# Optimization experiments

Hardware: AMD Instinct MI355X
Metric: run time of the kernel (lower is better)

## Reference

```python
import jax, jax.numpy as jnp
import numpy as np

B, C, H, W, NH = 8, 192, 128, 128, 6  # batch, channels, height, width, heads


def setup_inputs() -> dict:
    key = jax.random.key(0)
    ks = jax.random.split(key, 5)
    return {
        "x": jax.random.normal(ks[0], (B, C, H, W), jnp.float32),
        "w_qkv": jax.random.normal(ks[1], (3 * C, 1, 3, 3), jnp.float32) * 0.1,  # grouped conv, groups=C
        "b_qkv": jax.random.normal(ks[2], (3 * C,), jnp.float32) * 0.1,
        "temperature": jnp.ones((NH, 1, 1), jnp.float32),
        "w_out": jax.random.normal(ks[3], (C, C), jnp.float32) * 0.05,  # 1x1 conv as dense
        "b_out": jax.random.normal(ks[4], (C,), jnp.float32) * 0.05,
    }


def reference(x, w_qkv, b_qkv, temperature, w_out, b_out):
    b, c, h, w = x.shape
    nh = temperature.shape[0]
    # grouped 3x3 conv (groups = in_ch), padding=1
    qkv = jax.lax.conv_general_dilated(
        x, w_qkv, window_strides=(1, 1), padding=[(1, 1), (1, 1)],
        feature_group_count=c, dimension_numbers=("NCHW", "OIHW", "NCHW"),
    ) + b_qkv[None, :, None, None]
    q, k, v = jnp.split(qkv, 3, axis=1)  # each [b, c, h, w]

    def to_heads(t):
        return t.reshape(b, nh, c // nh, h * w)  # b head c (h w)

    q, k, v = to_heads(q), to_heads(k), to_heads(v)
    eps = 1e-12  # F.normalize default
    q = q / jnp.maximum(jnp.linalg.norm(q, axis=-1, keepdims=True), eps)
    k = k / jnp.maximum(jnp.linalg.norm(k, axis=-1, keepdims=True), eps)
    attn = jnp.einsum("bhcn,bhdn->bhcd", q, k) * temperature[None]  # [b, nh, c/nh, c/nh]
    attn = jax.nn.softmax(attn, axis=-1)
    out = jnp.einsum("bhcd,bhdn->bhcn", attn, v).reshape(b, c, h, w)
    out = jnp.einsum("oc,bchw->bohw", w_out, out) + b_out[None, :, None, None]
    return out
```

## Files before the change

### kernel.cpp

```cpp
#include <hip/hip_runtime.h>
#include <hip/hip_bf16.h>

constexpr int B   = 8;
constexpr int Cc  = 192;
constexpr int H   = 128;
constexpr int Wd  = 128;
constexpr int NH  = 6;
constexpr int HD  = 32;
constexpr int HW  = H * Wd;

typedef short s16x8 __attribute__((ext_vector_type(8)));
typedef float f32x16 __attribute__((ext_vector_type(16)));

constexpr size_t OFF_V    = 0;
constexpr size_t OFF_ATTN = 50331648ULL;
constexpr size_t OFF_SSQ  = OFF_ATTN + 196608ULL;
constexpr size_t OFF_ZERO = OFF_SSQ + 12288ULL;
constexpr size_t OFF_M    = OFF_ZERO + 256ULL;
constexpr int    N_ZERO   = (196608 + 12288 + 256) / 4;

__device__ inline unsigned short f2bf(float f) {
    __hip_bfloat16 h = __float2bfloat16(f);
    return *(unsigned short*)&h;
}

__global__ void zero_kernel(float* __restrict__ p, int n) {
    int i = blockIdx.x * 256 + threadIdx.x;
    if (i < n) p[i] = 0.f;
}

#define AS1C(p) ((const __attribute__((address_space(1))) void*)(p))
#define AS3(p)  ((__attribute__((address_space(3))) void*)(p))


__device__ __forceinline__ void ld6(const float* __restrict__ base, int r,
                                    int q8, float (&e)[6]) {
    const float* p = base + r * 40 + q8 * 4;
    float4 a = *(const float4*)p;
    float4 bq = *(const float4*)(p + 4);
    float2 cd = *(const float2*)(p + 8);
    e[0] = a.w; e[1] = bq.x; e[2] = bq.y; e[3] = bq.z; e[4] = bq.w; e[5] = cd.x;
}

__device__ __forceinline__ float conv_lds(
    const float* __restrict__ base, const float (&wr)[9], float br,
    int q8, int ch, unsigned short* __restrict__ frag)
{
    float rv[3][6];
    ld6(base, 0, q8, rv[0]);
    ld6(base, 1, q8, rv[1]);
    float ss = 0.f;
#pragma unroll
    for (int y = 0; y < 4; ++y) {
        ld6(base, y + 2, q8, rv[(y + 2) % 3]);
        const float* r0 = rv[y % 3];
        const float* r1 = rv[(y + 1) % 3];
        const float* r2 = rv[(y + 2) % 3];
        float o[4];
#pragma unroll
        for (int xx = 0; xx < 4; ++xx) {
            o[xx] = br
                + wr[0] * r0[xx] + wr[1] * r0[xx + 1] + wr[2] * r0[xx + 2]
                + wr[3] * r1[xx] + wr[4] * r1[xx + 1] + wr[5] * r1[xx + 2]
                + wr[6] * r2[xx] + wr[7] * r2[xx + 1] + wr[8] * r2[xx + 2];
        }
        ss += o[0] * o[0] + o[1] * o[1] + o[2] * o[2] + o[3] * o[3];
        ushort4 pk = make_ushort4(f2bf(o[0]), f2bf(o[1]), f2bf(o[2]), f2bf(o[3]));
        int g = 4 * y + (q8 >> 1);
        *(ushort4*)(frag + ((g * 32 + ch) << 3) + ((q8 & 1) << 2)) = pk;
    }
    return ss;
}

__global__ __launch_bounds__(256, 2) void fused_conv_qk(
    const float* __restrict__ x, const float* __restrict__ w,
    const float* __restrict__ bias, float* __restrict__ ssq,
    float* __restrict__ attn, const float* __restrict__ zbuf)
{
    const int tile = blockIdx.x, h = blockIdx.y, b = blockIdx.z;
    const int y0  = tile * 4;
    const int tid = threadIdx.x;
    const int ch  = tid >> 3, q8 = tid & 7;
    const int lane = tid & 63, wv = tid >> 6;
    const int m = lane & 31, hf = lane >> 5;

    __shared__ float xs[2][5760];
    __shared__ unsigned short qs[16 * 32 * 8];
    __shared__ unsigned short ks[16 * 32 * 8];

    const int gq0 = (h * 32) / 3;
    const int ncq = (h * 32 + 31) / 3 - gq0 + 1;
    const int gl  = (h * 32 + ch) / 3 - gq0;

    const int ocq = h * HD + ch;
    float wq[9], wk[9];
#pragma unroll
    for (int t = 0; t < 9; ++t) {
        wq[t] = w[(size_t)ocq * 9 + t];
        wk[t] = w[(size_t)(Cc + ocq) * 9 + t];
    }
    const float bq = bias[ocq], bk = bias[Cc + ocq];

    const float* sp[6];
    int cb[6];
    int i4[6];
    bool act[6];
#pragma unroll
    for (int j = 0; j < 6; ++j) {
        int i = tid + 256 * j;
        act[j] = (i < 1440);
        if (act[j]) {
            int t   = i / 720;
            int jj  = i - t * 720;
            int c   = jj / 60;
            int rem = jj - c * 60;
            int r   = rem / 10;
            int c4  = rem - r * 10;
            int cg  = (c < ncq) ? c : (ncq - 1);
            int gch = t * 64 + gq0 + cg;
            int y   = y0 - 1 + r;
            sp[j] = (y >= 0 && y < H)
                  ? x + ((size_t)b * Cc + gch) * HW + (size_t)y * Wd : nullptr;
            cb[j] = c4 * 4 - 4;
            i4[j] = i * 4;
        } else { sp[j] = nullptr; cb[j] = 0; i4[j] = 0; }
    }

    f32x16 acc;
#pragma unroll
    for (int i = 0; i < 16; ++i) acc[i] = 0.f;
    float ssq_a = 0.f, ssk_a = 0.f;

#pragma unroll
    for (int j = 0; j < 6; ++j) {
        if (!act[j]) continue;
        int col = cb[j];
        const float* src = (sp[j] != nullptr && (unsigned)col <= 124u)
                         ? sp[j] + col : zbuf;
        __builtin_amdgcn_global_load_lds(AS1C(src), AS3(&xs[0][i4[j]]), 16, 0, 0);
    }

#pragma unroll 1
    for (int s = 0; s < 4; ++s) {
        float* cur = xs[s & 1];
        __syncthreads();

        if (s < 3) {
            float* nxt = xs[(s + 1) & 1];
#pragma unroll
            for (int j = 0; j < 6; ++j) {
                if (!act[j]) continue;
                int col = (s + 1) * 32 + cb[j];
                const float* src = (sp[j] != nullptr && (unsigned)col <= 124u)
                                 ? sp[j] + col : zbuf;
                __builtin_amdgcn_global_load_lds(AS1C(src), AS3(&nxt[i4[j]]), 16, 0, 0);
            }
        }

        ssq_a += conv_lds(cur + gl * 240, wq, bq, q8, ch, qs);
        ssk_a += conv_lds(cur + 2880 + gl * 240, wk, bk, q8, ch, ks);
        __syncthreads();

#pragma unroll
        for (int cc = 0; cc < 2; ++cc) {
            int g = (wv * 2 + cc) * 2 + hf;
            s16x8 qa = *(const s16x8*)&qs[(g * 32 + m) << 3];
            s16x8 kb = *(const s16x8*)&ks[(g * 32 + m) << 3];
            acc = __builtin_amdgcn_mfma_f32_32x32x16_bf16(qa, kb, acc, 0, 0, 0);
        }
    }

    __syncthreads();
    float* sacc = (float*)qs;
    for (int i = tid; i < 1024; i += 256) sacc[i] = 0.f;
    __syncthreads();
#pragma unroll
    for (int r = 0; r < 16; ++r) {
        int row = (r & 3) + 8 * (r >> 2) + 4 * hf;
        atomicAdd(&sacc[row * 32 + m], acc[r]);
    }
    __syncthreads();
    float* ap = attn + (size_t)(b * NH + h) * 1024;
    for (int i = tid; i < 1024; i += 256) atomicAdd(&ap[i], sacc[i]);

    for (int off = 4; off; off >>= 1) {
        ssq_a += __shfl_down(ssq_a, off, 8);
        ssk_a += __shfl_down(ssk_a, off, 8);
    }
    if (q8 == 0) {
        atomicAdd(&ssq[b * Cc + ocq], ssq_a);
        atomicAdd(&ssq[B * Cc + b * Cc + ocq], ssk_a);
    }
}

constexpr int TS = 16;

__global__ __launch_bounds__(256) void conv_v(
    const float* __restrict__ x, const float* __restrict__ w,
    const float* __restrict__ bias, unsigned short* __restrict__ vws)
{
    int tile = blockIdx.x;
    int gv   = blockIdx.y;
    int b    = blockIdx.z;
    int y0   = tile * TS;

    __shared__ float sm[TS + 2][132];

    const float* xp = x + ((size_t)b * Cc + 128 + gv) * HW;
    for (int i = threadIdx.x; i < (TS + 2) * 32; i += 256) {
        int r = i >> 5, c4 = (i & 31) * 4;
        int y = y0 - 1 + r;
        if (y >= 0 && y < H) {
            float4 v4 = *(const float4*)(xp + (size_t)y * Wd + c4);
            sm[r][c4 + 1] = v4.x; sm[r][c4 + 2] = v4.y;
            sm[r][c4 + 3] = v4.z; sm[r][c4 + 4] = v4.w;
        } else {
            sm[r][c4 + 1] = 0.f; sm[r][c4 + 2] = 0.f;
            sm[r][c4 + 3] = 0.f; sm[r][c4 + 4] = 0.f;
        }
    }
    for (int i = threadIdx.x; i < (TS + 2) * 2; i += 256) {
        int r = i >> 1;
        sm[r][(i & 1) ? 129 : 0] = 0.f;
    }
    __syncthreads();

    float wreg[3][9], breg[3];
    for (int j = 0; j < 3; ++j) {
        const float* wp = w + (size_t)(2 * Cc + 3 * gv + j) * 9;
#pragma unroll
        for (int t = 0; t < 9; ++t) wreg[j][t] = wp[t];
        breg[j] = bias[2 * Cc + 3 * gv + j];
    }

    int xq = (threadIdx.x & 31) * 4;
    int ys = threadIdx.x >> 5;

    for (int yy = ys; yy < TS; yy += 8) {
        float rvv[3][6];
        for (int r = 0; r < 3; ++r) {
            float4 a4 = *(const float4*)&sm[yy + r][xq];
            float2 a2 = *(const float2*)&sm[yy + r][xq + 4];
            rvv[r][0] = a4.x; rvv[r][1] = a4.y; rvv[r][2] = a4.z;
            rvv[r][3] = a4.w; rvv[r][4] = a2.x; rvv[r][5] = a2.y;
        }
        for (int j = 0; j < 3; ++j) {
            unsigned short pk[4];
            for (int xx = 0; xx < 4; ++xx) {
                float s = breg[j]
                    + wreg[j][0] * rvv[0][xx] + wreg[j][1] * rvv[0][xx + 1] + wreg[j][2] * rvv[0][xx + 2]
                    + wreg[j][3] * rvv[1][xx] + wreg[j][4] * rvv[1][xx + 1] + wreg[j][5] * rvv[1][xx + 2]
                    + wreg[j][6] * rvv[2][xx] + wreg[j][7] * rvv[2][xx + 1] + wreg[j][8] * rvv[2][xx + 2];
                pk[xx] = f2bf(s);
            }
            unsigned short* op = vws + ((size_t)b * Cc + 3 * gv + j) * HW
                                     + (size_t)(y0 + yy) * Wd + xq;
            *(ushort4*)op = make_ushort4(pk[0], pk[1], pk[2], pk[3]);
        }
    }
}

__global__ void softmax_attn(float* __restrict__ attn,
                             const float* __restrict__ ssq,
                             const float* __restrict__ temp)
{
    int h = blockIdx.x % NH, b = blockIdx.x / NH;
    __shared__ float nk[32];
    if (threadIdx.x < 32)
        nk[threadIdx.x] = fmaxf(sqrtf(ssq[B * Cc + b * Cc + h * 32 + threadIdx.x]), 1e-12f);
    __syncthreads();
    int c = threadIdx.x;
    if (c >= 32) return;
    float nq = fmaxf(sqrtf(ssq[b * Cc + h * 32 + c]), 1e-12f);
    float t = temp[h];
    float* ap = attn + ((size_t)(b * NH + h) * 32 + c) * 32;
    float row[32];
    float mx = -1e30f;
    for (int d = 0; d < 32; ++d) {
        float v = ap[d] / (nq * nk[d]) * t;
        row[d] = v;
        mx = fmaxf(mx, v);
    }
    float sum = 0.f;
    for (int d = 0; d < 32; ++d) { row[d] = expf(row[d] - mx); sum += row[d]; }
    float inv = 1.f / sum;
    for (int d = 0; d < 32; ++d) ap[d] = row[d] * inv;
}

__global__ __launch_bounds__(256) void make_m(
    const float* __restrict__ attn, const float* __restrict__ w_out,
    unsigned short* __restrict__ M)
{
    int h = blockIdx.x, b = blockIdx.y;
    __shared__ float as[32][33];
    for (int i = threadIdx.x; i < 1024; i += 256)
        as[i / 32][i % 32] = attn[(size_t)((b * NH + h) * 32 + i / 32) * 32 + i % 32];
    __syncthreads();
    for (int i = threadIdx.x; i < Cc * 32; i += 256) {
        int o = i / 32, d = i % 32;
        const float* wp = w_out + (size_t)o * Cc + h * 32;
        float s = 0.f;
        for (int cp = 0; cp < 32; ++cp) s += wp[cp] * as[cp][d];
        M[((size_t)b * Cc + o) * Cc + h * 32 + d] = f2bf(s);
    }
}

constexpr int BN = 128;

__global__ __launch_bounds__(256) void out_gemm(
    const unsigned short* __restrict__ vws, const unsigned short* __restrict__ M,
    const float* __restrict__ b_out, float* __restrict__ out)
{
    int n0 = blockIdx.x * BN;
    int b  = blockIdx.y;

    const unsigned short* vp = vws + (size_t)b * Cc * HW;
    const unsigned short* mp = M + (size_t)b * Cc * Cc;

    __shared__ unsigned short vsT[BN][24];

    int tid  = threadIdx.x;
    int lane = tid & 63, wv = tid >> 6;
    int wm = wv & 1, wn = wv >> 1;
    int col = lane & 31, half = lane >> 5;

    f32x16 acc[6];
    for (int t = 0; t < 6; ++t)
        for (int i = 0; i < 16; ++i) acc[t][i] = 0.f;

    int p  = tid >> 5;
    int nq = tid & 31;

    const unsigned short* s0 = vp + (size_t)(2 * p) * HW + n0 + 4 * nq;
    ushort4 va = *(const ushort4*)s0;
    ushort4 vb = *(const ushort4*)(s0 + HW);

    for (int k0 = 0; k0 < Cc; k0 += 16) {
        *(unsigned int*)&vsT[4 * nq + 0][2 * p] = (unsigned int)va.x | ((unsigned int)vb.x << 16);
        *(unsigned int*)&vsT[4 * nq + 1][2 * p] = (unsigned int)va.y | ((unsigned int)vb.y << 16);
        *(unsigned int*)&vsT[4 * nq + 2][2 * p] = (unsigned int)va.z | ((unsigned int)vb.z << 16);
        *(unsigned int*)&vsT[4 * nq + 3][2 * p] = (unsigned int)va.w | ((unsigned int)vb.w << 16);
        __syncthreads();

        ushort4 va2 = make_ushort4(0, 0, 0, 0), vb2 = va2;
        if (k0 + 16 < Cc) {
            const unsigned short* s1 = vp + (size_t)(k0 + 16 + 2 * p) * HW + n0 + 4 * nq;
            va2 = *(const ushort4*)s1;
            vb2 = *(const ushort4*)(s1 + HW);
        }

        s16x8 af[3], bf[2];
        for (int mt = 0; mt < 3; ++mt) {
            int o = wm * 96 + mt * 32 + col;
            af[mt] = *(const s16x8*)(mp + (size_t)o * Cc + k0 + half * 8);
        }
        for (int nt = 0; nt < 2; ++nt) {
            int nn = wn * 64 + nt * 32 + col;
            bf[nt] = *(const s16x8*)&vsT[nn][half * 8];
        }
        for (int mt = 0; mt < 3; ++mt)
            for (int nt = 0; nt < 2; ++nt)
                acc[mt * 2 + nt] = __builtin_amdgcn_mfma_f32_32x32x16_bf16(
                    af[mt], bf[nt], acc[mt * 2 + nt], 0, 0, 0);
        __syncthreads();
        va = va2; vb = vb2;
    }

    for (int mt = 0; mt < 3; ++mt)
        for (int nt = 0; nt < 2; ++nt) {
            f32x16 c = acc[mt * 2 + nt];
            int n = n0 + wn * 64 + nt * 32 + col;
            for (int r = 0; r < 16; ++r) {
                int row = (r & 3) + 8 * (r >> 2) + 4 * half;
                int o = wm * 96 + mt * 32 + row;
                out[((size_t)b * Cc + o) * HW + n] = c[r] + b_out[o];
            }
        }
}

extern "C" void kernel_launch(void* const* d_in, const int* in_sizes, int n_in,
                              void* d_out, int out_size, void* d_ws, size_t ws_size,
                              hipStream_t stream) {
    const float* x      = (const float*)d_in[0];
    const float* w_qkv  = (const float*)d_in[1];
    const float* b_qkv  = (const float*)d_in[2];
    const float* temp   = (const float*)d_in[3];
    const float* w_out  = (const float*)d_in[4];
    const float* b_out  = (const float*)d_in[5];
    float* out = (float*)d_out;

    char* ws = (char*)d_ws;
    unsigned short* vws = (unsigned short*)(ws + OFF_V);
    float* attn         = (float*)(ws + OFF_ATTN);
    float* ssq          = (float*)(ws + OFF_SSQ);
    const float* zbuf   = (const float*)(ws + OFF_ZERO);
    unsigned short* M   = (unsigned short*)(ws + OFF_M);

    zero_kernel<<<(N_ZERO + 255) / 256, 256, 0, stream>>>(attn, N_ZERO);
    fused_conv_qk<<<dim3(H / 4, NH, B), 256, 0, stream>>>(x, w_qkv, b_qkv, ssq, attn, zbuf);
    conv_v<<<dim3(H / TS, 64, B), 256, 0, stream>>>(x, w_qkv, b_qkv, vws);
    softmax_attn<<<B * NH, 64, 0, stream>>>(attn, ssq, temp);
    make_m<<<dim3(NH, B), 256, 0, stream>>>(attn, w_out, M);
    out_gemm<<<dim3(HW / BN, B), 256, 0, stream>>>(vws, M, b_out, out);
}
```

Baseline: 292.7 us.

## Stage full V tile into LDS via direct global-to-LDS loads in out_gemm

The output GEMM now loads the whole 192x128 bf16 V tile into shared memory once, using global_load_lds direct-to-LDS transfers, in place of a per-k-step register transpose with a barrier on every step. The B fragments are then gathered with scalar LDS reads, and the main loop runs with no synchronisation. Launch bounds request 3 blocks per SM and the loops are unrolled. The cost is a much larger LDS footprint (48KB) and eight 2-byte LDS reads per fragment, which may cause bank conflicts and limit occupancy.

```diff
diff --git a/kernel.cpp b/kernel.cpp
--- a/kernel.cpp
+++ b/kernel.cpp
@@ -307,7 +307,7 @@
 
 constexpr int BN = 128;
 
-__global__ __launch_bounds__(256) void out_gemm(
+__global__ __launch_bounds__(256, 3) void out_gemm(
     const unsigned short* __restrict__ vws, const unsigned short* __restrict__ M,
     const float* __restrict__ b_out, float* __restrict__ out)
 {
@@ -317,63 +317,70 @@
     const unsigned short* vp = vws + (size_t)b * Cc * HW;
     const unsigned short* mp = M + (size_t)b * Cc * Cc;
 
-    __shared__ unsigned short vsT[BN][24];
+    __shared__ unsigned short vs[Cc][BN];
 
     int tid  = threadIdx.x;
     int lane = tid & 63, wv = tid >> 6;
     int wm = wv & 1, wn = wv >> 1;
     int col = lane & 31, half = lane >> 5;
 
+    {
+        int c0 = wv * 48;
+        const unsigned short* sb = vp + (size_t)(c0 + (lane >> 4)) * HW
+                                      + n0 + (lane & 15) * 8;
+#pragma unroll
+        for (int t = 0; t < 12; ++t) {
+            __builtin_amdgcn_global_load_lds(AS1C(sb + (size_t)(4 * t) * HW),
+                                             AS3(&vs[c0 + 4 * t][0]), 16, 0, 0);
+        }
+    }
+    __syncthreads();
+
     f32x16 acc[6];
+#pragma unroll
     for (int t = 0; t < 6; ++t)
+#pragma unroll
         for (int i = 0; i < 16; ++i) acc[t][i] = 0.f;
 
-    int p  = tid >> 5;
-    int nq = tid & 31;
-
-    const unsigned short* s0 = vp + (size_t)(2 * p) * HW + n0 + 4 * nq;
-    ushort4 va = *(const ushort4*)s0;
-    ushort4 vb = *(const ushort4*)(s0 + HW);
-
+    const int nn0 = wn * 64 + col;
+    const unsigned short* mrow[3];
+#pragma unroll
+    for (int mt = 0; mt < 3; ++mt)
+        mrow[mt] = mp + (size_t)(wm * 96 + mt * 32 + col) * Cc + half * 8;
+
+#pragma unroll 2
     for (int k0 = 0; k0 < Cc; k0 += 16) {
-        *(unsigned int*)&vsT[4 * nq + 0][2 * p] = (unsigned int)va.x | ((unsigned int)vb.x << 16);
-        *(unsigned int*)&vsT[4 * nq + 1][2 * p] = (unsigned int)va.y | ((unsigned int)vb.y << 16);
-        *(unsigned int*)&vsT[4 * nq + 2][2 * p] = (unsigned int)va.z | ((unsigned int)vb.z << 16);
-        *(unsigned int*)&vsT[4 * nq + 3][2 * p] = (unsigned int)va.w | ((unsigned int)vb.w << 16);
-        __syncthreads();
-
-        ushort4 va2 = make_ushort4(0, 0, 0, 0), vb2 = va2;
-        if (k0 + 16 < Cc) {
-            const unsigned short* s1 = vp + (size_t)(k0 + 16 + 2 * p) * HW + n0 + 4 * nq;
-            va2 = *(const ushort4*)s1;
-            vb2 = *(const ushort4*)(s1 + HW);
-        }
-
-        s16x8 af[3], bf[2];
+        s16x8 af[3];
+#pragma unroll
+        for (int mt = 0; mt < 3; ++mt)
+            af[mt] = *(const s16x8*)(mrow[mt] + k0);
+
+        union { s16x8 v8; unsigned short u[8]; } b0, b1;
+#pragma unroll
+        for (int j = 0; j < 8; ++j) {
+            b0.u[j] = vs[k0 + half * 8 + j][nn0];
+            b1.u[j] = vs[k0 + half * 8 + j][nn0 + 32];
+        }
+
+#pragma unroll
         for (int mt = 0; mt < 3; ++mt) {
-            int o = wm * 96 + mt * 32 + col;
-            af[mt] = *(const s16x8*)(mp + (size_t)o * Cc + k0 + half * 8);
-        }
+            acc[mt * 2 + 0] = __builtin_amdgcn_mfma_f32_32x32x16_bf16(
+                af[mt], b0.v8, acc[mt * 2 + 0], 0, 0, 0);
+            acc[mt * 2 + 1] = __builtin_amdgcn_mfma_f32_32x32x16_bf16(
+                af[mt], b1.v8, acc[mt * 2 + 1], 0, 0, 0);
+        }
+    }
+
+#pragma unroll
+    for (int mt = 0; mt < 3; ++mt)
+#pragma unroll
         for (int nt = 0; nt < 2; ++nt) {
-            int nn = wn * 64 + nt * 32 + col;
-            bf[nt] = *(const s16x8*)&vsT[nn][half * 8];
-        }
-        for (int mt = 0; mt < 3; ++mt)
-            for (int nt = 0; nt < 2; ++nt)
-                acc[mt * 2 + nt] = __builtin_amdgcn_mfma_f32_32x32x16_bf16(
-                    af[mt], bf[nt], acc[mt * 2 + nt], 0, 0, 0);
-        __syncthreads();
-        va = va2; vb = vb2;
-    }
-
-    for (int mt = 0; mt < 3; ++mt)
-        for (int nt = 0; nt < 2; ++nt) {
-            f32x16 c = acc[mt * 2 + nt];
             int n = n0 + wn * 64 + nt * 32 + col;
+#pragma unroll
             for (int r = 0; r < 16; ++r) {
                 int row = (r & 3) + 8 * (r >> 2) + 4 * half;
                 int o = wm * 96 + mt * 32 + row;
-                out[((size_t)b * Cc + o) * HW + n] = c[r] + b_out[o];
+                out[((size_t)b * Cc + o) * HW + n] = acc[mt * 2 + nt][r] + b_out[o];
             }
         }
 }
```

New measurement: 293.5 us. About the same (+0.3%).
